# Kernel optimization log

Measured on AMD Instinct MI355X. Metric: run time of the kernel, lower is better.

Reference implementation:

```python
import jax, jax.numpy as jnp
import numpy as np
from jax.ops import segment_sum

N_NODES = 300000
N_EDGES = 600000
N_GRAPHS = 12000
HIDDEN = 128
F_ATOM, V_ATOM, D_ATOM = 9, 119, 9
F_BOND, V_BOND, D_BOND = 3, 6, 3


def setup_inputs() -> dict:
    key = jax.random.key(0)
    ks = jax.random.split(key, 12)
    x = jax.random.randint(ks[0], (N_NODES, F_ATOM), 0, 100, dtype=jnp.int64 if jax.config.jax_enable_x64 else jnp.int32)
    edge_index = jax.random.randint(ks[1], (2, N_EDGES), 0, N_NODES)
    edge_attr = jax.random.randint(ks[2], (N_EDGES, F_BOND), 0, 5)
    batch = jnp.sort(jax.random.randint(ks[3], (N_NODES,), 0, N_GRAPHS))
    s = 0.02
    atom_emb = jax.random.normal(ks[4], (F_ATOM, V_ATOM, D_ATOM), jnp.float32) * s
    bond_emb = jax.random.normal(ks[5], (F_BOND, V_BOND, D_BOND), jnp.float32) * s
    W1 = jax.random.normal(ks[6], (D_ATOM, HIDDEN), jnp.float32) * (1.0 / np.sqrt(D_ATOM))
    b1 = jnp.zeros((HIDDEN,), jnp.float32)
    W2 = jax.random.normal(ks[7], (HIDDEN, HIDDEN), jnp.float32) * (1.0 / np.sqrt(HIDDEN))
    b2 = jnp.zeros((HIDDEN,), jnp.float32)
    Wfc = jax.random.normal(ks[8], (HIDDEN, 128), jnp.float32) * (1.0 / np.sqrt(HIDDEN))
    bfc = jnp.zeros((128,), jnp.float32)
    return {"x": x, "edge_index": edge_index, "edge_attr": edge_attr, "batch": batch,
            "atom_emb": atom_emb, "bond_emb": bond_emb,
            "W1": W1, "b1": b1, "W2": W2, "b2": b2, "Wfc": Wfc, "bfc": bfc}


def _multi_embed(tables, idx):
    # tables: [F, V, D], idx: [N, F] -> sum over F of tables[f, idx[:, f]] -> [N, D]
    F = tables.shape[0]
    gathered = tables[jnp.arange(F)[None, :], idx]  # [N, F, D]
    return gathered.sum(axis=1)


def _gcn_conv(h, edge_index, W, b, n_nodes):
    # PyG GCNConv: add self-loops, symmetric deg^-1/2 normalization
    src, dst = edge_index[0], edge_index[1]
    deg = segment_sum(jnp.ones(src.shape[0], h.dtype), dst, num_segments=n_nodes) + 1.0  # self-loop
    dinv = jax.lax.rsqrt(deg)
    h = h @ W  # transform before propagation
    coef = (dinv[src] * dinv[dst])[:, None]
    agg = segment_sum(h[src] * coef, dst, num_segments=n_nodes)
    agg = agg + h * (dinv * dinv)[:, None]  # self-loop contribution (norm = 1/deg)
    return agg + b


def reference(x, edge_index, edge_attr, batch, atom_emb, bond_emb, W1, b1, W2, b2, Wfc, bfc):
    h = _multi_embed(atom_emb, x)            # AtomEncoder: [N, 9]
    _ = _multi_embed(bond_emb, edge_attr)    # BondEncoder (computed, unused downstream)
    h = _gcn_conv(h, edge_index, W1, b1, N_NODES)
    h = jax.nn.relu(h)
    h = _gcn_conv(h, edge_index, W2, b2, N_NODES)
    # global_mean_pool over graphs
    sums = segment_sum(h, batch, num_segments=N_GRAPHS)
    cnt = segment_sum(jnp.ones(N_NODES, h.dtype), batch, num_segments=N_GRAPHS)
    graph_emb = sums / jnp.clip(cnt, 1.0)[:, None]
    return graph_emb @ Wfc + bfc
```

## Files before the change

### kernel.cpp

```cpp
#include <hip/hip_runtime.h>

#define NN 300000
#define NE 600000
#define NG 12000
#define HH 128
#define FA 9
#define VA 119
#define DA 9
#define NCHUNK ((NN + 1023) / 1024)

#define OEMB 0
#define OW1  (FA*VA*DA)
#define OB1  (OW1 + DA*HH)
#define OW2  (OB1 + HH)
#define OB2  (OW2 + HH*HH)
#define OWFC (OB2 + HH)
#define OBFC (OWFC + HH*HH)
#define NWC  (OBFC + HH)

typedef unsigned short u16;
typedef unsigned int u32;
typedef __attribute__((ext_vector_type(8))) short bfrag8;
typedef __attribute__((ext_vector_type(4))) float ffrag4;

__device__ __forceinline__ float bf2f(u16 u){
  union { u32 i; float f; } v; v.i = ((u32)u) << 16; return v.f;
}
__device__ __forceinline__ float bflo(u32 w){
  union { u32 i; float f; } v; v.i = w << 16; return v.f;
}
__device__ __forceinline__ float bfhi(u32 w){
  union { u32 i; float f; } v; v.i = w & 0xFFFF0000u; return v.f;
}
__device__ __forceinline__ u16 f2bf(float f){
  union { float f; u32 i; } v; v.f = f;
  u32 x = v.i;
  return (u16)((x + 0x7FFFu + ((x >> 16) & 1u)) >> 16);
}
__device__ __forceinline__ float ldf(const void* p, int i, int isf32){
  return isf32 ? ((const float*)p)[i] : bf2f(((const u16*)p)[i]);
}
__device__ __forceinline__ int detect_isf32(const u16* emb16, int t, int* scnt){
  if (t == 0) *scnt = 0;
  __syncthreads();
  u16 u = emb16[t];
  int e = (u >> 7) & 0xFF;
  if (e >= 96 && e < 126) atomicAdd(scnt, 1);
  __syncthreads();
  return (*scnt >= 200) ? 0 : 1;
}

__global__ void k_pre(const int* __restrict__ x, const void* emb, const void* W1,
                      const void* b1, const void* W2, const void* b2,
                      const void* Wfc, const void* bfc,
                      const int* __restrict__ batch, const int* __restrict__ dst,
                      int* __restrict__ flag, float* __restrict__ wc,
                      int* __restrict__ degcur, u16* __restrict__ rank,
                      int* __restrict__ gstart, uint4* __restrict__ h0a,
                      u32* __restrict__ h0b, float* __restrict__ wcomb,
                      float* __restrict__ bcomb, u32* __restrict__ btab){
  __shared__ float embS[FA * VA * DA];
  __shared__ int scnt;
  int t = threadIdx.x;
  int isf32 = detect_isf32((const u16*)emb, t, &scnt);
  int tid = blockIdx.x * 256 + t;
  int nth = gridDim.x * 256;
  if (tid == 0) flag[0] = isf32;

  {
    int e0 = tid * 2;
    if (e0 < NE){
      int r0 = atomicAdd(&degcur[dst[e0]], 1);
      rank[e0] = (u16)r0;
    }
    if (e0 + 1 < NE){
      int r1 = atomicAdd(&degcur[dst[e0 + 1]], 1);
      rank[e0 + 1] = (u16)r1;
    }
  }

  for (int i = t; i < FA * VA * DA; i += 256) embS[i] = ldf(emb, i, isf32);
  for (int i = tid; i < NWC; i += nth){
    float v;
    if      (i < OW1)  v = ldf(emb, i - OEMB, isf32);
    else if (i < OB1)  v = ldf(W1,  i - OW1,  isf32);
    else if (i < OW2)  v = ldf(b1,  i - OB1,  isf32);
    else if (i < OB2)  v = ldf(W2,  i - OW2,  isf32);
    else if (i < OWFC) v = ldf(b2,  i - OB2,  isf32);
    else if (i < OBFC) v = ldf(Wfc, i - OWFC, isf32);
    else               v = ldf(bfc, i - OBFC, isf32);
    wc[i] = v;
  }

  if (tid < HH * HH){
    int d = tid >> 7, k = tid & 127;
    float s = 0.f;
    #pragma unroll 4
    for (int j = 0; j < HH; ++j) s += ldf(W2, d * HH + j, isf32) * ldf(Wfc, j * HH + k, isf32);
    wcomb[tid] = s;
    if (tid < HH){
      float sb = 0.f;
      #pragma unroll 4
      for (int j = 0; j < HH; ++j) sb += ldf(b2, j, isf32) * ldf(Wfc, j * HH + tid, isf32);
      bcomb[tid] = sb;
    }
    if (tid < 2048){
      int lane = tid >> 5, idx = tid & 31;
      int tile = idx >> 2, reg = idx & 3;
      int kq = lane >> 4, li = lane & 15;
      int nn = tile * 16 + li;
      int k0 = kq * 8 + reg * 2;
      int k1 = k0 + 1;
      u32 lo = 0, hi = 0;
      if (k0 < 9)       lo = f2bf(ldf(W1, k0 * HH + nn, isf32));
      else if (k0 == 9) lo = f2bf(ldf(b1, nn, isf32));
      if (k1 < 9)       hi = f2bf(ldf(W1, k1 * HH + nn, isf32));
      else if (k1 == 9) hi = f2bf(ldf(b1, nn, isf32));
      btab[tid] = lo | (hi << 16);
    }
  }

  __syncthreads();
  int n = tid;
  if (n <= NG){
    if (n == NG) gstart[NG] = NN;
    else {
      int lo = 0, hi = NN;
      while (lo < hi){
        int mid = (lo + hi) >> 1;
        if (batch[mid] < n) lo = mid + 1; else hi = mid;
      }
      gstart[n] = lo;
    }
  }
  if (n >= NN) return;
  int idx[FA];
  #pragma unroll
  for (int f = 0; f < FA; ++f) idx[f] = x[n * FA + f];
  float acc[DA];
  #pragma unroll
  for (int d = 0; d < DA; ++d){
    float a = 0.f;
    #pragma unroll
    for (int f = 0; f < FA; ++f) a += embS[(f * VA + idx[f]) * DA + d];
    acc[d] = a;
  }
  uint4 pv;
  pv.x = (u32)f2bf(acc[0]) | ((u32)f2bf(acc[1]) << 16);
  pv.y = (u32)f2bf(acc[2]) | ((u32)f2bf(acc[3]) << 16);
  pv.z = (u32)f2bf(acc[4]) | ((u32)f2bf(acc[5]) << 16);
  pv.w = (u32)f2bf(acc[6]) | ((u32)f2bf(acc[7]) << 16);
  h0a[n] = pv;
  h0b[n] = (u32)f2bf(acc[8]);
}

__global__ void k_scan1(const int* __restrict__ deg, int* __restrict__ rowoff,
                        int* __restrict__ part){
  __shared__ int sh[256];
  int base = blockIdx.x * 1024;
  int t = threadIdx.x;
  int i0 = base + t * 4;
  int v0=0, v1=0, v2=0, v3=0;
  if (i0 + 0 < NN) v0 = deg[i0 + 0];
  if (i0 + 1 < NN) v1 = deg[i0 + 1];
  if (i0 + 2 < NN) v2 = deg[i0 + 2];
  if (i0 + 3 < NN) v3 = deg[i0 + 3];
  int tsum = v0 + v1 + v2 + v3;
  sh[t] = tsum;
  __syncthreads();
  for (int off = 1; off < 256; off <<= 1){
    int add = (t >= off) ? sh[t - off] : 0;
    __syncthreads();
    sh[t] += add;
    __syncthreads();
  }
  int run = sh[t] - tsum;
  if (t == 255) part[blockIdx.x] = sh[255];
  if (i0 + 0 < NN){ rowoff[i0 + 0] = run; run += v0; }
  if (i0 + 1 < NN){ rowoff[i0 + 1] = run; run += v1; }
  if (i0 + 2 < NN){ rowoff[i0 + 2] = run; run += v2; }
  if (i0 + 3 < NN){ rowoff[i0 + 3] = run; run += v3; }
}

__global__ void k_scan3(const int* __restrict__ deg, int* __restrict__ rowoff,
                        float* __restrict__ dinv, const int* __restrict__ part){
  __shared__ int red[256];
  int t = threadIdx.x;
  int c = blockIdx.x >> 2;
  int acc = 0;
  for (int j = t; j < c; j += 256) acc += part[j];
  red[t] = acc;
  __syncthreads();
  for (int off = 128; off > 0; off >>= 1){
    if (t < off) red[t] += red[t + off];
    __syncthreads();
  }
  int P = red[0];
  int i = blockIdx.x * 256 + t;
  if (i < NN){
    rowoff[i] = rowoff[i] + P;
    dinv[i] = rsqrtf((float)deg[i] + 1.0f);
  }
  if (i == 0) rowoff[NN] = NE;
}

__global__ void k_fill(const int* __restrict__ src, const int* __restrict__ dst,
                       const u16* __restrict__ rank, const int* __restrict__ rowoff,
                       const float* __restrict__ dinv, uint2* __restrict__ csr){
  int e = blockIdx.x * 256 + threadIdx.x;
  if (e < NE){
    int s = src[e], d = dst[e];
    int pos = rowoff[d] + (int)rank[e];
    uint2 ent;
    ent.x = (u32)s;
    ent.y = __float_as_uint(dinv[s] * dinv[d]);
    csr[pos] = ent;
  }
}

__global__ void k_l1csr(const uint4* __restrict__ h0a, const u32* __restrict__ h0b,
                        uint4* __restrict__ agg1a, u32* __restrict__ agg1b,
                        const int* __restrict__ rowoff, const uint2* __restrict__ csr,
                        const float* __restrict__ dinv){
  int n = blockIdx.x * 256 + threadIdx.x;
  if (n >= NN) return;
  float di = dinv[n];
  float c0 = di * di;
  float acc[DA];
  {
    uint4 ra = h0a[n];
    u32 r4 = h0b[n];
    acc[0]=c0*bflo(ra.x); acc[1]=c0*bfhi(ra.x); acc[2]=c0*bflo(ra.y); acc[3]=c0*bfhi(ra.y);
    acc[4]=c0*bflo(ra.z); acc[5]=c0*bfhi(ra.z); acc[6]=c0*bflo(ra.w); acc[7]=c0*bfhi(ra.w);
    acc[8]=c0*bflo(r4);
  }
  int s0 = rowoff[n], s1 = rowoff[n + 1];
  #pragma unroll 2
  for (int j = s0; j < s1; ++j){
    uint2 ent = csr[j];
    int s = (int)ent.x;
    float c = __uint_as_float(ent.y);
    uint4 ra = h0a[s];
    u32 r4 = h0b[s];
    acc[0]+=c*bflo(ra.x); acc[1]+=c*bfhi(ra.x); acc[2]+=c*bflo(ra.y); acc[3]+=c*bfhi(ra.y);
    acc[4]+=c*bflo(ra.z); acc[5]+=c*bfhi(ra.z); acc[6]+=c*bflo(ra.w); acc[7]+=c*bfhi(ra.w);
    acc[8]+=c*bflo(r4);
  }
  uint4 pv;
  pv.x = (u32)f2bf(acc[0]) | ((u32)f2bf(acc[1]) << 16);
  pv.y = (u32)f2bf(acc[2]) | ((u32)f2bf(acc[3]) << 16);
  pv.z = (u32)f2bf(acc[4]) | ((u32)f2bf(acc[5]) << 16);
  pv.w = (u32)f2bf(acc[6]) | ((u32)f2bf(acc[7]) << 16);
  agg1a[n] = pv;
  agg1b[n] = (u32)f2bf(acc[8]) | (0x3F80u << 16);
}

__global__ void k_l2pool(const uint4* __restrict__ agg1a, const u32* __restrict__ agg1b,
                         const float* __restrict__ dinv,
                         const int* __restrict__ rowoff, const uint2* __restrict__ csr,
                         const int* __restrict__ gstart, const u32* __restrict__ btab,
                         float* __restrict__ pooled){
  int t = threadIdx.x;
  int g = blockIdx.x * 4 + (t >> 6);
  int lane = t & 63;
  if (g >= NG) return;
  u32 bf[32];
  {
    const u32* bp = btab + lane * 32;
    #pragma unroll
    for (int i = 0; i < 32; ++i) bf[i] = bp[i];
  }
  int a = gstart[g], b = gstart[g + 1];
  int j0 = rowoff[a], j1 = rowoff[b];
  int nself = b - a;
  int M = nself + (j1 - j0);
  float s[8];
  #pragma unroll
  for (int i = 0; i < 8; ++i) s[i] = 0.f;
  int kq = lane >> 4, li = lane & 15;

  for (int base = 0; base < M; base += 16){
    u32 a0 = 0, a1 = 0, a2 = 0, a3 = 0;
    float coef = 0.f;
    int i = base + li;
    if (kq < 2 && i < M){
      int n;
      if (i < nself){
        n = a + i;
        float dn = dinv[n];
        coef = dn * dn;
      } else {
        uint2 e = csr[j0 + (i - nself)];
        n = (int)e.x;
        coef = __uint_as_float(e.y);
      }
      if (kq == 0){
        uint4 ra = agg1a[n];
        a0 = ra.x; a1 = ra.y; a2 = ra.z; a3 = ra.w;
      } else {
        a0 = agg1b[n];
      }
    }
    float cv0 = __shfl(coef, kq * 4 + 0, 64);
    float cv1 = __shfl(coef, kq * 4 + 1, 64);
    float cv2 = __shfl(coef, kq * 4 + 2, 64);
    float cv3 = __shfl(coef, kq * 4 + 3, 64);
    union { u32 u[4]; bfrag8 v; } au;
    au.u[0] = a0; au.u[1] = a1; au.u[2] = a2; au.u[3] = a3;
    #pragma unroll
    for (int tile = 0; tile < 8; ++tile){
      union { u32 u[4]; bfrag8 v; } bu;
      bu.u[0] = bf[tile*4+0]; bu.u[1] = bf[tile*4+1];
      bu.u[2] = bf[tile*4+2]; bu.u[3] = bf[tile*4+3];
      ffrag4 c = {0.f, 0.f, 0.f, 0.f};
      c = __builtin_amdgcn_mfma_f32_16x16x32_bf16(au.v, bu.v, c, 0, 0, 0);
      s[tile] += fmaxf(c[0], 0.f) * cv0 + fmaxf(c[1], 0.f) * cv1
               + fmaxf(c[2], 0.f) * cv2 + fmaxf(c[3], 0.f) * cv3;
    }
  }
  #pragma unroll
  for (int tile = 0; tile < 8; ++tile){
    float v = s[tile];
    v += __shfl_xor(v, 16, 64);
    v += __shfl_xor(v, 32, 64);
    s[tile] = v;
  }
  if (kq == 0){
    #pragma unroll
    for (int tile = 0; tile < 8; ++tile)
      pooled[(size_t)g * HH + tile * 16 + li] = s[tile];
  }
}

__global__ void k_head(const float* __restrict__ pooled, const float* __restrict__ wcomb,
                       const float* __restrict__ bcomb, const float* __restrict__ wc,
                       const int* __restrict__ gstart, const int* __restrict__ flag,
                       void* __restrict__ out){
  __shared__ float wS[HH * HH];
  __shared__ float pl[2][HH];
  int t = threadIdx.x;
  for (int i = t; i < HH * HH; i += 256) wS[i] = wcomb[i];
  __syncthreads();
  int isf32 = flag[0];
  int gg = t >> 7, k = t & 127;
  for (int p = blockIdx.x; p < NG / 2; p += gridDim.x){
    int g = p * 2 + gg;
    int cnt = gstart[g + 1] - gstart[g];
    float inv = 1.0f / (float)(cnt > 1 ? cnt : 1);
    pl[gg][k] = pooled[(size_t)g * HH + k] * inv;
    __syncthreads();
    float acc = wc[OBFC + k] + (cnt > 0 ? bcomb[k] : 0.f);
    #pragma unroll 8
    for (int d = 0; d < HH; ++d) acc += pl[gg][d] * wS[d * HH + k];
    if (isf32) ((float*)out)[(size_t)g * HH + k] = acc;
    else       ((u16*)out)[(size_t)g * HH + k] = f2bf(acc);
    __syncthreads();
  }
}

extern "C" void kernel_launch(void* const* d_in, const int* in_sizes, int n_in,
                              void* d_out, int out_size, void* d_ws, size_t ws_size,
                              hipStream_t stream){
  const int* x     = (const int*)d_in[0];
  const int* ei    = (const int*)d_in[1];
  const int* batch = (const int*)d_in[3];
  const void* aemb = d_in[4];
  const void* W1   = d_in[6];
  const void* b1   = d_in[7];
  const void* W2   = d_in[8];
  const void* b2   = d_in[9];
  const void* Wfc  = d_in[10];
  const void* bfc  = d_in[11];
  const int* srcp = ei;
  const int* dstp = ei + NE;

  char* p = (char*)d_ws;
  int*   flag   = (int*)p;                 p += 64;
  float* wc     = (float*)p;               p += sizeof(float) * 43944;
  float* wcomb  = (float*)p;               p += sizeof(float) * (HH * HH);
  float* bcomb  = (float*)p;               p += sizeof(float) * HH;
  u32*   btab   = (u32*)p;                 p += sizeof(u32) * 2048;
  int*   degcur = (int*)p;                 p += sizeof(int) * (NN + 16);
  int*   rowoff = (int*)p;                 p += sizeof(int) * (NN + 4);
  int*   part   = (int*)p;                 p += sizeof(int) * 512;
  float* dinv   = (float*)p;               p += sizeof(float) * NN;
  u16*   rank   = (u16*)p;                 p += sizeof(u16) * (NE + 8);
  uint2* csr    = (uint2*)p;               p += sizeof(uint2) * NE;
  int*   gstart = (int*)p;                 p += sizeof(int) * (NG + 4);
  float* pooled = (float*)p;               p += sizeof(float) * (size_t)NG * HH;
  uint4* h0a    = (uint4*)p;               p += sizeof(uint4) * NN;
  u32*   h0b    = (u32*)p;                 p += sizeof(u32) * NN;
  uint4* agg1a  = (uint4*)p;               p += sizeof(uint4) * NN;
  u32*   agg1b  = (u32*)p;                 p += sizeof(u32) * NN;
  (void)p; (void)ws_size; (void)n_in; (void)in_sizes; (void)out_size;

  hipMemsetAsync(degcur, 0, sizeof(int) * (NN + 16), stream);
  k_pre   <<<(NN + 255) / 256, 256, 0, stream>>>(x, aemb, W1, b1, W2, b2, Wfc, bfc,
                                                 batch, dstp, flag, wc, degcur, rank,
                                                 gstart, h0a, h0b, wcomb, bcomb, btab);
  k_scan1 <<<NCHUNK, 256, 0, stream>>>(degcur, rowoff, part);
  k_scan3 <<<(NN + 255) / 256, 256, 0, stream>>>(degcur, rowoff, dinv, part);
  k_fill  <<<(NE + 255) / 256, 256, 0, stream>>>(srcp, dstp, rank, rowoff, dinv, csr);
  k_l1csr <<<(NN + 255) / 256, 256, 0, stream>>>(h0a, h0b, agg1a, agg1b, rowoff, csr, dinv);
  k_l2pool<<<NG / 4, 256, 0, stream>>>(agg1a, agg1b, dinv, rowoff, csr, gstart, btab, pooled);
  k_head  <<<1500, 256, 0, stream>>>(pooled, wcomb, bcomb, wc, gstart, flag, d_out);
}
```

Baseline: 255.1 us.

## Fuse head GEMM into layer-2 pooling and replace scan fixup with tiny block-offset scan

Two changes. The degree scan drops the per-element fixup pass: a single-block scan now turns the per-chunk partials into block offsets, and consumers add the chunk offset when they read rowoff. The pooling kernel now also does the final projection itself, keeping pooled means in shared memory instead of writing them to global and launching a separate head kernel. This removes a global round trip of the pooled matrix and one or two launches, but every pooling block now loads the full 64KB weight matrix into LDS, which may lower occupancy.

```diff
diff --git a/kernel.cpp b/kernel.cpp
--- a/kernel.cpp
+++ b/kernel.cpp
@@ -155,16 +155,16 @@
 }
 
 __global__ void k_scan1(const int* __restrict__ deg, int* __restrict__ rowoff,
-                        int* __restrict__ part){
+                        float* __restrict__ dinv, int* __restrict__ part){
   __shared__ int sh[256];
   int base = blockIdx.x * 1024;
   int t = threadIdx.x;
   int i0 = base + t * 4;
   int v0=0, v1=0, v2=0, v3=0;
-  if (i0 + 0 < NN) v0 = deg[i0 + 0];
-  if (i0 + 1 < NN) v1 = deg[i0 + 1];
-  if (i0 + 2 < NN) v2 = deg[i0 + 2];
-  if (i0 + 3 < NN) v3 = deg[i0 + 3];
+  if (i0 + 0 < NN){ v0 = deg[i0 + 0]; dinv[i0 + 0] = rsqrtf((float)v0 + 1.0f); }
+  if (i0 + 1 < NN){ v1 = deg[i0 + 1]; dinv[i0 + 1] = rsqrtf((float)v1 + 1.0f); }
+  if (i0 + 2 < NN){ v2 = deg[i0 + 2]; dinv[i0 + 2] = rsqrtf((float)v2 + 1.0f); }
+  if (i0 + 3 < NN){ v3 = deg[i0 + 3]; dinv[i0 + 3] = rsqrtf((float)v3 + 1.0f); }
   int tsum = v0 + v1 + v2 + v3;
   sh[t] = tsum;
   __syncthreads();
@@ -176,41 +176,40 @@
   }
   int run = sh[t] - tsum;
   if (t == 255) part[blockIdx.x] = sh[255];
-  if (i0 + 0 < NN){ rowoff[i0 + 0] = run; run += v0; }
-  if (i0 + 1 < NN){ rowoff[i0 + 1] = run; run += v1; }
-  if (i0 + 2 < NN){ rowoff[i0 + 2] = run; run += v2; }
-  if (i0 + 3 < NN){ rowoff[i0 + 3] = run; run += v3; }
-}
-
-__global__ void k_scan3(const int* __restrict__ deg, int* __restrict__ rowoff,
-                        float* __restrict__ dinv, const int* __restrict__ part){
-  __shared__ int red[256];
+  if (i0 + 0 <= NN) rowoff[i0 + 0] = run;
+  run += v0;
+  if (i0 + 1 <= NN) rowoff[i0 + 1] = run;
+  run += v1;
+  if (i0 + 2 <= NN) rowoff[i0 + 2] = run;
+  run += v2;
+  if (i0 + 3 <= NN) rowoff[i0 + 3] = run;
+}
+
+__global__ void k_scan2(int* __restrict__ part){
+  __shared__ int sh[512];
   int t = threadIdx.x;
-  int c = blockIdx.x >> 2;
-  int acc = 0;
-  for (int j = t; j < c; j += 256) acc += part[j];
-  red[t] = acc;
-  __syncthreads();
-  for (int off = 128; off > 0; off >>= 1){
-    if (t < off) red[t] += red[t + off];
+  int v = (t < NCHUNK) ? part[t] : 0;
+  sh[t] = v;
+  __syncthreads();
+  for (int off = 1; off < 512; off <<= 1){
+    int add = (t >= off) ? sh[t - off] : 0;
     __syncthreads();
-  }
-  int P = red[0];
-  int i = blockIdx.x * 256 + t;
-  if (i < NN){
-    rowoff[i] = rowoff[i] + P;
-    dinv[i] = rsqrtf((float)deg[i] + 1.0f);
-  }
-  if (i == 0) rowoff[NN] = NE;
-}
+    sh[t] += add;
+    __syncthreads();
+  }
+  if (t < NCHUNK) part[t] = sh[t] - v;
+}
+
+#define GROW(i) (rowoff[(i)] + part[(u32)(i) >> 10])
 
 __global__ void k_fill(const int* __restrict__ src, const int* __restrict__ dst,
                        const u16* __restrict__ rank, const int* __restrict__ rowoff,
-                       const float* __restrict__ dinv, uint2* __restrict__ csr){
+                       const int* __restrict__ part, const float* __restrict__ dinv,
+                       uint2* __restrict__ csr){
   int e = blockIdx.x * 256 + threadIdx.x;
   if (e < NE){
     int s = src[e], d = dst[e];
-    int pos = rowoff[d] + (int)rank[e];
+    int pos = GROW(d) + (int)rank[e];
     uint2 ent;
     ent.x = (u32)s;
     ent.y = __float_as_uint(dinv[s] * dinv[d]);
@@ -220,8 +219,8 @@
 
 __global__ void k_l1csr(const uint4* __restrict__ h0a, const u32* __restrict__ h0b,
                         uint4* __restrict__ agg1a, u32* __restrict__ agg1b,
-                        const int* __restrict__ rowoff, const uint2* __restrict__ csr,
-                        const float* __restrict__ dinv){
+                        const int* __restrict__ rowoff, const int* __restrict__ part,
+                        const uint2* __restrict__ csr, const float* __restrict__ dinv){
   int n = blockIdx.x * 256 + threadIdx.x;
   if (n >= NN) return;
   float di = dinv[n];
@@ -234,7 +233,7 @@
     acc[4]=c0*bflo(ra.z); acc[5]=c0*bfhi(ra.z); acc[6]=c0*bflo(ra.w); acc[7]=c0*bfhi(ra.w);
     acc[8]=c0*bflo(r4);
   }
-  int s0 = rowoff[n], s1 = rowoff[n + 1];
+  int s0 = GROW(n), s1 = GROW(n + 1);
   #pragma unroll 2
   for (int j = s0; j < s1; ++j){
     uint2 ent = csr[j];
@@ -255,15 +254,21 @@
   agg1b[n] = (u32)f2bf(acc[8]) | (0x3F80u << 16);
 }
 
-__global__ void k_l2pool(const uint4* __restrict__ agg1a, const u32* __restrict__ agg1b,
+__global__ void k_l2head(const uint4* __restrict__ agg1a, const u32* __restrict__ agg1b,
                          const float* __restrict__ dinv,
-                         const int* __restrict__ rowoff, const uint2* __restrict__ csr,
-                         const int* __restrict__ gstart, const u32* __restrict__ btab,
-                         float* __restrict__ pooled){
+                         const int* __restrict__ rowoff, const int* __restrict__ part,
+                         const uint2* __restrict__ csr, const int* __restrict__ gstart,
+                         const u32* __restrict__ btab, const float* __restrict__ wcomb,
+                         const float* __restrict__ bcomb, const float* __restrict__ wc,
+                         const int* __restrict__ flag, void* __restrict__ out){
+  __shared__ float wS[HH * HH];
+  __shared__ float pmS[4][HH];
   int t = threadIdx.x;
+  for (int i = t; i < HH * HH; i += 256) wS[i] = wcomb[i];
+
   int g = blockIdx.x * 4 + (t >> 6);
+  int slot = t >> 6;
   int lane = t & 63;
-  if (g >= NG) return;
   u32 bf[32];
   {
     const u32* bp = btab + lane * 32;
@@ -271,7 +276,7 @@
     for (int i = 0; i < 32; ++i) bf[i] = bp[i];
   }
   int a = gstart[g], b = gstart[g + 1];
-  int j0 = rowoff[a], j1 = rowoff[b];
+  int j0 = GROW(a), j1 = GROW(b);
   int nself = b - a;
   int M = nself + (j1 - j0);
   float s[8];
@@ -325,36 +330,31 @@
     v += __shfl_xor(v, 32, 64);
     s[tile] = v;
   }
+  float inv = 1.0f / (float)(nself > 1 ? nself : 1);
   if (kq == 0){
     #pragma unroll
     for (int tile = 0; tile < 8; ++tile)
-      pooled[(size_t)g * HH + tile * 16 + li] = s[tile];
-  }
-}
-
-__global__ void k_head(const float* __restrict__ pooled, const float* __restrict__ wcomb,
-                       const float* __restrict__ bcomb, const float* __restrict__ wc,
-                       const int* __restrict__ gstart, const int* __restrict__ flag,
-                       void* __restrict__ out){
-  __shared__ float wS[HH * HH];
-  __shared__ float pl[2][HH];
-  int t = threadIdx.x;
-  for (int i = t; i < HH * HH; i += 256) wS[i] = wcomb[i];
-  __syncthreads();
+      pmS[slot][tile * 16 + li] = s[tile] * inv;
+  }
+  __syncthreads();
+
   int isf32 = flag[0];
-  int gg = t >> 7, k = t & 127;
-  for (int p = blockIdx.x; p < NG / 2; p += gridDim.x){
-    int g = p * 2 + gg;
-    int cnt = gstart[g + 1] - gstart[g];
-    float inv = 1.0f / (float)(cnt > 1 ? cnt : 1);
-    pl[gg][k] = pooled[(size_t)g * HH + k] * inv;
-    __syncthreads();
-    float acc = wc[OBFC + k] + (cnt > 0 ? bcomb[k] : 0.f);
-    #pragma unroll 8
-    for (int d = 0; d < HH; ++d) acc += pl[gg][d] * wS[d * HH + k];
-    if (isf32) ((float*)out)[(size_t)g * HH + k] = acc;
-    else       ((u16*)out)[(size_t)g * HH + k] = f2bf(acc);
-    __syncthreads();
+  int k = lane * 2;
+  float acc0 = wc[OBFC + k]     + (nself > 0 ? bcomb[k]     : 0.f);
+  float acc1 = wc[OBFC + k + 1] + (nself > 0 ? bcomb[k + 1] : 0.f);
+  #pragma unroll 8
+  for (int d = 0; d < HH; ++d){
+    float pmd = pmS[slot][d];
+    float2 w = *(const float2*)&wS[d * HH + k];
+    acc0 += pmd * w.x;
+    acc1 += pmd * w.y;
+  }
+  if (isf32){
+    float2 o; o.x = acc0; o.y = acc1;
+    ((float2*)((float*)out + (size_t)g * HH))[lane] = o;
+  } else {
+    u32 o = (u32)f2bf(acc0) | ((u32)f2bf(acc1) << 16);
+    ((u32*)((u16*)out + (size_t)g * HH))[lane] = o;
   }
 }
 
@@ -387,7 +387,6 @@
   u16*   rank   = (u16*)p;                 p += sizeof(u16) * (NE + 8);
   uint2* csr    = (uint2*)p;               p += sizeof(uint2) * NE;
   int*   gstart = (int*)p;                 p += sizeof(int) * (NG + 4);
-  float* pooled = (float*)p;               p += sizeof(float) * (size_t)NG * HH;
   uint4* h0a    = (uint4*)p;               p += sizeof(uint4) * NN;
   u32*   h0b    = (u32*)p;                 p += sizeof(u32) * NN;
   uint4* agg1a  = (uint4*)p;               p += sizeof(uint4) * NN;
@@ -398,10 +397,10 @@
   k_pre   <<<(NN + 255) / 256, 256, 0, stream>>>(x, aemb, W1, b1, W2, b2, Wfc, bfc,
                                                  batch, dstp, flag, wc, degcur, rank,
                                                  gstart, h0a, h0b, wcomb, bcomb, btab);
-  k_scan1 <<<NCHUNK, 256, 0, stream>>>(degcur, rowoff, part);
-  k_scan3 <<<(NN + 255) / 256, 256, 0, stream>>>(degcur, rowoff, dinv, part);
-  k_fill  <<<(NE + 255) / 256, 256, 0, stream>>>(srcp, dstp, rank, rowoff, dinv, csr);
-  k_l1csr <<<(NN + 255) / 256, 256, 0, stream>>>(h0a, h0b, agg1a, agg1b, rowoff, csr, dinv);
-  k_l2pool<<<NG / 4, 256, 0, stream>>>(agg1a, agg1b, dinv, rowoff, csr, gstart, btab, pooled);
-  k_head  <<<1500, 256, 0, stream>>>(pooled, wcomb, bcomb, wc, gstart, flag, d_out);
-}
+  k_scan1 <<<NCHUNK, 256, 0, stream>>>(degcur, rowoff, dinv, part);
+  k_scan2 <<<1, 512, 0, stream>>>(part);
+  k_fill  <<<(NE + 255) / 256, 256, 0, stream>>>(srcp, dstp, rank, rowoff, part, dinv, csr);
+  k_l1csr <<<(NN + 255) / 256, 256, 0, stream>>>(h0a, h0b, agg1a, agg1b, rowoff, part, csr, dinv);
+  k_l2head<<<NG / 4, 256, 0, stream>>>(agg1a, agg1b, dinv, rowoff, part, csr, gstart,
+                                       btab, wcomb, bcomb, wc, flag, d_out);
+}
```

After: 269.3 us. 1.06x slower.
